# Kernel tuning notes

Hardware: AMD Instinct MI355X
Metric: run time of the kernel (lower is better)

Reference implementation:

```python
import jax, jax.numpy as jnp
import numpy as np

C, S, K, SIGMA = 512, 11, 3, 16
B = 128
EPS = 1e-5  # BatchNorm eps (eval mode, running_mean=0, running_var=1)


def _make_dct_weight(Cc, H, W):
    # FcaNet 'low16' frequency selection
    lx = [0, 0, 1, 1, 0, 2, 2, 1, 2, 0, 3, 4, 0, 1, 3, 0]
    ly = [0, 1, 0, 1, 2, 0, 1, 2, 2, 3, 0, 0, 4, 3, 1, 5]
    mx = [u * (H // 7) for u in lx]
    my = [v * (W // 7) for v in ly]
    w = np.zeros((Cc, H, W), np.float32)
    cp = Cc // len(lx)

    def bf(pos, freq, POS):
        r = np.cos(np.pi * freq * (pos + 0.5) / POS) / np.sqrt(POS)
        return r if freq == 0 else r * np.sqrt(2.0)

    for i, (u, v) in enumerate(zip(mx, my)):
        for tx in range(H):
            for ty in range(W):
                w[i * cp:(i + 1) * cp, tx, ty] = bf(tx, u, H) * bf(ty, v, W)
    return jnp.asarray(w)


def _bn(f, g, b):
    # eval-mode BatchNorm2d: (f - 0)/sqrt(1+eps)*g + b, per channel (axis 1)
    s = g / jnp.sqrt(1.0 + EPS)
    return f * s[None, :, None, None] + b[None, :, None, None]


def _conv1x1(f, w, b):
    return jnp.einsum('bchw,oc->bohw', f, w) + b[None, :, None, None]


def _spatial_kernel(f, w_conv, b_conv, g_sp, b_sp):
    Bn = f.shape[0]
    s = _conv1x1(f, w_conv, b_conv)                  # (B, K*K, S, S)
    s = s.reshape(Bn, K * K, S * S).transpose(0, 2, 1)  # (B, S*S, K*K)
    s = _bn(s.reshape(Bn, S * S, K, K), g_sp, b_sp)
    return s.reshape(Bn, S * S, K * K)


def _channel_kernel(f, dct_w, fc1, fc2, g_ch, b_ch):
    y = jnp.sum(f * dct_w[None], axis=(-2, -1))      # (B, C) DCT pooling
    y = jax.nn.sigmoid(jax.nn.relu(y @ fc1.T) @ fc2.T)  # (B, C*K*K)
    y = _bn(y.reshape(-1, C, K, K), g_ch, b_ch)
    return y.reshape(-1, C, K * K)


def _unfold(f):
    # torch-style per-pixel kxk neighborhoods -> (B, C, H, W, K, K)
    p = (K + 1) // 2 - 1
    Bn, Cn, H, W = f.shape
    fp = jnp.pad(f, ((0, 0), (0, 0), (p, p), (p, p)))
    pat = jnp.stack([fp[:, :, di:di + H, dj:dj + W]
                     for di in range(K) for dj in range(K)], axis=-1)
    return pat.reshape(Bn, Cn, H, W, K, K)


def setup_inputs() -> dict:
    key = jax.random.key(0)
    ks = iter(jax.random.split(key, 32))

    def nrm(shape, s=0.02):
        return s * jax.random.normal(next(ks), shape, jnp.float32)

    def gma(shape):
        return 1.0 + 0.1 * jax.random.normal(next(ks), shape, jnp.float32)

    return dict(
        x=jax.random.normal(next(ks), (B, C, S, S), jnp.float32),
        dct_w=_make_dct_weight(C, S, S),
        w_conv=nrm((K * K, C)), b_conv=nrm((K * K,)),
        g_sp=gma((S * S,)), b_sp=nrm((S * S,), 0.05),
        g_ch=gma((C,)), b_ch=nrm((C,), 0.05),
        fc1=nrm((C // SIGMA, C)), fc2=nrm((C * K * K, C // SIGMA)),
        up_w1=nrm((2 * C, C)), up_b1=nrm((2 * C,)), up_g1=gma((2 * C,)), up_bb1=nrm((2 * C,), 0.05),
        up_w2=nrm((2 * C, 2 * C)), up_b2=nrm((2 * C,)), up_g2=gma((2 * C,)), up_bb2=nrm((2 * C,), 0.05),
        lo_w1=nrm((2 * C, 2 * C)), lo_b1=nrm((2 * C,)), lo_g1=gma((2 * C,)), lo_bb1=nrm((2 * C,), 0.05),
        lo_w2=nrm((C, 2 * C)), lo_b2=nrm((C,)), lo_g2=gma((C,)), lo_bb2=nrm((C,), 0.05),
    )


def reference(x, dct_w, w_conv, b_conv, g_sp, b_sp, g_ch, b_ch, fc1, fc2,
              up_w1, up_b1, up_g1, up_bb1, up_w2, up_b2, up_g2, up_bb2,
              lo_w1, lo_b1, lo_g1, lo_bb1, lo_w2, lo_b2, lo_g2, lo_bb2):
    Bn = x.shape[0]
    # instance kernel: spatial (B,1,HW,KK) x channel (B,C,1,KK)
    sk = _spatial_kernel(x, w_conv, b_conv, g_sp, b_sp)[:, None]
    ck = _channel_kernel(x, dct_w, fc1, fc2, g_ch, b_ch)[:, :, None]
    inst = (sk * ck).reshape(Bn, C, S, S, K, K)
    # CLM task representation (sum over batch between upper and lower)
    a = jax.nn.relu(_bn(_conv1x1(x, up_w1, up_b1), up_g1, up_bb1))
    a = jax.nn.relu(_bn(_conv1x1(a, up_w2, up_b2), up_g2, up_bb2))
    a = a.sum(axis=0, keepdims=True)
    a = jax.nn.relu(_bn(_conv1x1(a, lo_w1, lo_b1), lo_g1, lo_bb1))
    task_s = jax.nn.sigmoid(_bn(_conv1x1(a, lo_w2, lo_b2), lo_g2, lo_bb2))
    # task kernel (shared across the batch)
    sk_t = _spatial_kernel(task_s, w_conv, b_conv, g_sp, b_sp)[:, None]
    ck_t = _channel_kernel(task_s, dct_w, fc1, fc2, g_ch, b_ch)[:, :, None]
    task_kernel = (sk_t * ck_t).reshape(1, C, S, S, K, K)
    kernel = task_kernel * inst
    adapted = (_unfold(x) * kernel).mean(axis=(-1, -2))  # (B,C,S,S)
    return adapted + x, task_kernel
```

## Files before the change

### kernel.cpp

```cpp
#include <hip/hip_runtime.h>
#include <hip/hip_bf16.h>
#include <math.h>

#define BNEPS 1e-5f
#define BDIM_B 128
#define CDIM 512
#define SS 121
#define KK 9
#define MROWS (BDIM_B * SS)

typedef unsigned short u16;
typedef __bf16 bf16x8 __attribute__((ext_vector_type(8)));
typedef float f32x4 __attribute__((ext_vector_type(4)));

__device__ __forceinline__ u16 f2bf(float f) {
    union { float f; unsigned int u; } v; v.f = f;
    unsigned int r = v.u + 0x7FFF + ((v.u >> 16) & 1);
    return (u16)(r >> 16);
}
__device__ __forceinline__ float bf2f(u16 v) {
    union { unsigned int u; float f; } x; x.u = ((unsigned int)v) << 16; return x.f;
}

__device__ __forceinline__ void gld16(const u16* g, u16* l) {
    __builtin_amdgcn_global_load_lds(
        (const __attribute__((address_space(1))) void*)g,
        (__attribute__((address_space(3))) void*)l, 16, 0, 0);
}

template<int MODE, int SWIZ>
__global__ __launch_bounds__(256)
void gemm_mfma(const u16* __restrict__ A, const u16* __restrict__ Bw,
               const float* __restrict__ bias, const float* __restrict__ g,
               const float* __restrict__ bb, void* __restrict__ out,
               int Kd, int N, int NT)
{
    __shared__ __align__(16) u16 Als[2][128 * 32];
    __shared__ __align__(16) u16 Bls[2][128 * 32];

    const int tid  = threadIdx.x;
    const int lane = tid & 63;
    const int w    = tid >> 6;
    const int wm   = w >> 1, wn = w & 1;

    int bx, by;
    if (SWIZ) {
        int i = blockIdx.x;
        if (i < 960) {
            int xg = i & 7;
            int j  = i >> 3;
            bx = xg * 15 + (j >> 3);
            by = j & 7;
        } else { bx = 120; by = i - 960; }
    } else {
        bx = blockIdx.x / NT; by = blockIdx.x - bx * NT;
    }
    const int bm = bx * 128;
    const int bn = by * 128;

    f32x4 acc[4][4] = {};

    const int subrow = tid >> 2;
    const int kq     = tid & 3;
    const int gchunk = kq ^ ((subrow >> 1) & 3);
    const u16* Ab = A  + (size_t)(bm + subrow) * Kd + gchunk * 8;
    const u16* Bb = Bw + (size_t)(bn + subrow) * Kd + gchunk * 8;
    u16* Al0  = &Als[0][(w * 16) * 32];
    u16* Al1  = &Als[0][(w * 16 + 64) * 32];
    u16* Bl0  = &Bls[0][(w * 16) * 32];
    u16* Bl1  = &Bls[0][(w * 16 + 64) * 32];
    u16* Al0b = &Als[1][(w * 16) * 32];
    u16* Al1b = &Als[1][(w * 16 + 64) * 32];
    u16* Bl0b = &Bls[1][(w * 16) * 32];
    u16* Bl1b = &Bls[1][(w * 16 + 64) * 32];

    const int fa_row = wm * 64 + (lane & 15);
    const int fb_row = wn * 64 + (lane & 15);
    const int kofs   = (((lane >> 4) ^ (((lane & 15) >> 1) & 3))) * 8;

    for (int k0 = 0; k0 < Kd; k0 += 64) {
        __syncthreads();
        gld16(Ab + k0,                      Al0);
        gld16(Ab + (size_t)64 * Kd + k0,    Al1);
        gld16(Bb + k0,                      Bl0);
        gld16(Bb + (size_t)64 * Kd + k0,    Bl1);
        gld16(Ab + k0 + 32,                 Al0b);
        gld16(Ab + (size_t)64 * Kd + k0 + 32, Al1b);
        gld16(Bb + k0 + 32,                 Bl0b);
        gld16(Bb + (size_t)64 * Kd + k0 + 32, Bl1b);
        __syncthreads();

        #pragma unroll
        for (int hb = 0; hb < 2; ++hb) {
            const u16* Ah = &Als[hb][0];
            const u16* Bh = &Bls[hb][0];
            bf16x8 af[4], bfv[4];
            #pragma unroll
            for (int i = 0; i < 4; ++i)
                af[i] = *(const bf16x8*)&Ah[(fa_row + i * 16) * 32 + kofs];
            #pragma unroll
            for (int j = 0; j < 4; ++j)
                bfv[j] = *(const bf16x8*)&Bh[(fb_row + j * 16) * 32 + kofs];
            #pragma unroll
            for (int i = 0; i < 4; ++i)
                #pragma unroll
                for (int j = 0; j < 4; ++j)
                    acc[i][j] = __builtin_amdgcn_mfma_f32_16x16x32_bf16(af[i], bfv[j], acc[i][j], 0, 0, 0);
        }
    }

    const float inv = 1.0f / sqrtf(1.0f + BNEPS);

    if (MODE == 1) {
        u16* Y = (u16*)out;
        int dstrow[4][4];
        #pragma unroll
        for (int i = 0; i < 4; ++i) {
            int mb = bm + wm * 64 + i * 16 + (lane >> 4) * 4;
            #pragma unroll
            for (int r = 0; r < 4; ++r) {
                int m = mb + r;
                int b = m / 121, p = m - b * 121;
                dstrow[i][r] = p * 128 + b;
            }
        }
        #pragma unroll
        for (int j = 0; j < 4; ++j) {
            int n = bn + wn * 64 + j * 16 + (lane & 15);
            float sc = g[n] * inv, bo = bias[n], bv = bb[n];
            #pragma unroll
            for (int i = 0; i < 4; ++i)
                #pragma unroll
                for (int r = 0; r < 4; ++r) {
                    float v = (acc[i][j][r] + bo) * sc + bv;
                    v = fmaxf(v, 0.0f);
                    Y[(size_t)dstrow[i][r] * N + n] = f2bf(v);
                }
        }
    } else {
        float ps[4];
        #pragma unroll
        for (int j = 0; j < 4; ++j) {
            int n = bn + wn * 64 + j * 16 + (lane & 15);
            float sc = g[n] * inv, bo = bias[n], bv = bb[n];
            float s = 0.f;
            #pragma unroll
            for (int i = 0; i < 4; ++i)
                #pragma unroll
                for (int r = 0; r < 4; ++r) {
                    float v = (acc[i][j][r] + bo) * sc + bv;
                    s += fmaxf(v, 0.0f);
                }
            ps[j] = s;
        }
        __syncthreads();
        float* red = (float*)Als;
        #pragma unroll
        for (int j = 0; j < 4; ++j)
            red[(wm * 4 + (lane >> 4)) * 128 + wn * 64 + j * 16 + (lane & 15)] = ps[j];
        __syncthreads();
        if (tid < 128) {
            float s = 0.f;
            #pragma unroll
            for (int r = 0; r < 8; ++r) s += red[r * 128 + tid];
            ((u16*)out)[(size_t)bx * N + bn + tid] = f2bf(s);
        }
    }
}

template<int MODE>
__global__ __launch_bounds__(256)
void gemm_small(const u16* __restrict__ A, const u16* __restrict__ Bw,
                const float* __restrict__ bias, const float* __restrict__ g,
                const float* __restrict__ bb, u16* __restrict__ Y,
                int Kd, int N)
{
    const int bn   = blockIdx.x * 64;
    const int tid  = threadIdx.x;
    const int lane = tid & 63;
    const int w    = tid >> 6;
    const int fr   = lane & 15;
    const int kq   = lane >> 4;
    const int r0   = w * 32;

    f32x4 acc[2][4] = {};
    const u16* a0p = A + (size_t)(r0 + fr) * Kd + kq * 8;
    const u16* a1p = a0p + (size_t)16 * Kd;
    const u16* bp  = Bw + (size_t)(bn + fr) * Kd + kq * 8;

    #pragma unroll 4
    for (int k0 = 0; k0 < Kd; k0 += 32) {
        bf16x8 a0 = *(const bf16x8*)(a0p + k0);
        bf16x8 a1 = *(const bf16x8*)(a1p + k0);
        #pragma unroll
        for (int j = 0; j < 4; ++j) {
            bf16x8 bv = *(const bf16x8*)(bp + (size_t)j * 16 * Kd + k0);
            acc[0][j] = __builtin_amdgcn_mfma_f32_16x16x32_bf16(a0, bv, acc[0][j], 0, 0, 0);
            acc[1][j] = __builtin_amdgcn_mfma_f32_16x16x32_bf16(a1, bv, acc[1][j], 0, 0, 0);
        }
    }

    const float inv = 1.0f / sqrtf(1.0f + BNEPS);
    #pragma unroll
    for (int j = 0; j < 4; ++j) {
        int n = bn + j * 16 + (lane & 15);
        float sc = g[n] * inv, bo = bias[n], bv = bb[n];
        #pragma unroll
        for (int t = 0; t < 2; ++t)
            #pragma unroll
            for (int r = 0; r < 4; ++r) {
                int m = r0 + t * 16 + (lane >> 4) * 4 + r;
                float v = (acc[t][j][r] + bo) * sc + bv;
                if (MODE == 3) v = fmaxf(v, 0.0f);
                else           v = 1.f / (1.f + expf(-v));
                Y[(size_t)m * N + n] = f2bf(v);
            }
    }
}

__device__ __forceinline__ void spatial_body(
    const u16* __restrict__ Arow, const u16* __restrict__ wcb,
    const float* __restrict__ b_conv, const float* __restrict__ g_sp,
    const float* __restrict__ b_sp, float* __restrict__ skb,
    bool task, int blk, float* __restrict__ skt)
{
    const float inv = 1.0f / sqrtf(1.0f + BNEPS);
    const int tid  = threadIdx.x;
    const int lane = tid & 63;
    const int w    = tid >> 6;
    const int fr   = lane & 15;
    const int kq   = lane >> 4;
    const int r0   = w * 32;

    f32x4 acc0 = {}, acc1 = {};
    const u16* a0p = Arow + (size_t)(r0 + fr) * 512 + kq * 8;
    const u16* a1p = a0p + (size_t)16 * 512;
    const u16* bp  = wcb + (size_t)fr * 512 + kq * 8;
    #pragma unroll
    for (int k0 = 0; k0 < 512; k0 += 32) {
        bf16x8 a0 = *(const bf16x8*)(a0p + k0);
        bf16x8 a1 = *(const bf16x8*)(a1p + k0);
        bf16x8 b  = *(const bf16x8*)(bp + k0);
        acc0 = __builtin_amdgcn_mfma_f32_16x16x32_bf16(a0, b, acc0, 0, 0, 0);
        acc1 = __builtin_amdgcn_mfma_f32_16x16x32_bf16(a1, b, acc1, 0, 0, 0);
    }

    int n = lane & 15;
    if (n < 9) {
        float bo = b_conv[n];
        #pragma unroll
        for (int t = 0; t < 2; ++t) {
            f32x4 a = t ? acc1 : acc0;
            #pragma unroll
            for (int r = 0; r < 4; ++r) {
                int mloc = r0 + t * 16 + (lane >> 4) * 4 + r;
                if (!task) {
                    int m = blk * 128 + mloc;
                    int p = m % 121;
                    float v = (a[r] + bo) * (g_sp[p] * inv) + b_sp[p];
                    skb[(size_t)m * 9 + n] = v;
                } else if (mloc < 121) {
                    float v = (a[r] + bo) * (g_sp[mloc] * inv) + b_sp[mloc];
                    skt[(size_t)mloc * 9 + n] = v;
                }
            }
        }
    }
}

__device__ __forceinline__ void channel_body(
    const u16* __restrict__ src, const float* __restrict__ dctT,
    const float* __restrict__ fc1, const float* __restrict__ fc2,
    const float* __restrict__ g_ch, const float* __restrict__ b_ch,
    float* __restrict__ outp, float* yls, float* y2ls)
{
    const float inv = 1.0f / sqrtf(1.0f + BNEPS);

    {
        int c = threadIdx.x * 2;
        float s0 = 0.f, s1 = 0.f;
        for (int p = 0; p < SS; ++p) {
            unsigned v = *(const unsigned*)(src + (size_t)p * 512 + c);
            float2 d  = *(const float2*)(dctT + (size_t)p * 512 + c);
            s0 += bf2f((u16)(v & 0xFFFFu)) * d.x;
            s1 += bf2f((u16)(v >> 16)) * d.y;
        }
        yls[c] = s0; yls[c + 1] = s1;
    }
    __syncthreads();

    {
        int o = threadIdx.x >> 3, kp = threadIdx.x & 7;
        const float* w = fc1 + (size_t)o * 512;
        float s = 0.f;
        for (int k = kp * 4; k < 512; k += 32) {
            float4 wv = *(const float4*)(w + k);
            float4 av = *(const float4*)(yls + k);
            s += wv.x * av.x + wv.y * av.y + wv.z * av.z + wv.w * av.w;
        }
        s += __shfl_xor(s, 1);
        s += __shfl_xor(s, 2);
        s += __shfl_xor(s, 4);
        if (kp == 0) y2ls[o] = fmaxf(s, 0.f);
    }
    __syncthreads();

    for (int o = threadIdx.x; o < CDIM * KK; o += 256) {
        const float* w = fc2 + (size_t)o * 32;
        float s = 0.f;
        #pragma unroll
        for (int k = 0; k < 32; ++k) s += y2ls[k] * w[k];
        s = 1.f / (1.f + expf(-s));
        int c = o / KK;
        s = s * (g_ch[c] * inv) + b_ch[c];
        outp[o] = s;
    }
}

__global__ __launch_bounds__(256)
void spatial_ck_combo(const u16* __restrict__ Xb, const u16* __restrict__ Xt,
                      const u16* __restrict__ wcb, const float* __restrict__ b_conv,
                      const float* __restrict__ g_sp, const float* __restrict__ b_sp,
                      const float* __restrict__ dctT,
                      const float* __restrict__ fc1, const float* __restrict__ fc2,
                      const float* __restrict__ g_ch, const float* __restrict__ b_ch,
                      float* __restrict__ skb, float* __restrict__ skt,
                      float* __restrict__ ckbuf, float* __restrict__ ck_t)
{
    __shared__ float sm[544];
    if (blockIdx.x < 122) {
        const bool task = (blockIdx.x == 121);
        spatial_body(task ? Xt : Xb + (size_t)blockIdx.x * 128 * 512,
                     wcb, b_conv, g_sp, b_sp, skb, task, blockIdx.x, skt);
        return;
    }
    const int g = blockIdx.x - 122;
    const u16* src = (g < 128) ? Xb + (size_t)g * 121 * 512 : Xt;
    channel_body(src, dctT, fc1, fc2, g_ch, b_ch,
                 (g < 128) ? ckbuf + (size_t)g * CDIM * KK : ck_t, sm, sm + 512);
}

#define W1N (1024 * 512)
#define W2N (1024 * 1024)
#define L1N (1024 * 1024)
#define L2N (512 * 1024)
#define VECN ((W1N + W2N + L1N + L2N) / 4)
#define DCTN (512 * 121)
#define WCN (16 * 512)
#define PREP_ELEM (VECN + DCTN + WCN)
#define PREP_BLKS (1024 + (PREP_ELEM + 255) / 256)
__global__ void prep_combo(const float* __restrict__ x, u16* __restrict__ Xb,
                           const float* __restrict__ w1, const float* __restrict__ w2,
                           const float* __restrict__ l1, const float* __restrict__ l2,
                           const float* __restrict__ dct, const float* __restrict__ w_conv,
                           u16* __restrict__ o1, u16* __restrict__ o2,
                           u16* __restrict__ o3, u16* __restrict__ o4,
                           float* __restrict__ dctT, u16* __restrict__ wcb)
{
    __shared__ float t[64 * 121];
    if (blockIdx.x < 1024) {
        int b = blockIdx.x >> 3, c0 = (blockIdx.x & 7) * 64;
        for (int idx = threadIdx.x; idx < 64 * 121; idx += 256) {
            int c = idx / 121, p = idx - c * 121;
            t[idx] = x[((size_t)b * 512 + c0 + c) * 121 + p];
        }
        __syncthreads();
        for (int idx = threadIdx.x; idx < 121 * 64; idx += 256) {
            int p = idx >> 6, c = idx & 63;
            Xb[((size_t)(b * 121 + p)) * 512 + c0 + c] = f2bf(t[c * 121 + p]);
        }
        return;
    }
    int i = (blockIdx.x - 1024) * 256 + threadIdx.x;
    if (i < VECN) {
        int q = i;
        const float* s; u16* d;
        if (q < W1N / 4)                    { s = w1; d = o1; }
        else if (q < (W1N + W2N) / 4)       { s = w2; d = o2; q -= W1N / 4; }
        else if (q < (W1N + W2N + L1N) / 4) { s = l1; d = o3; q -= (W1N + W2N) / 4; }
        else                                { s = l2; d = o4; q -= (W1N + W2N + L1N) / 4; }
        float4 v = ((const float4*)s)[q];
        uint2 r;
        r.x = (unsigned)f2bf(v.x) | ((unsigned)f2bf(v.y) << 16);
        r.y = (unsigned)f2bf(v.z) | ((unsigned)f2bf(v.w) << 16);
        ((uint2*)d)[q] = r;
        return;
    }
    i -= VECN;
    if (i < DCTN) {
        int p = i >> 9, c = i & 511;
        dctT[i] = dct[(size_t)c * 121 + p];
        return;
    }
    i -= DCTN;
    if (i < WCN) {
        int n = i >> 9, c = i & 511;
        wcb[i] = (n < 9) ? f2bf(w_conv[(size_t)n * 512 + c]) : (u16)0;
    }
}

#define TKN (CDIM * SS * KK)
#define FIN_BLKS (1024 + (TKN + 255) / 256)
__global__ __launch_bounds__(256)
void final_combo(const float* __restrict__ x, const float* __restrict__ skb,
                 const float* __restrict__ sk_t, const float* __restrict__ ckbuf,
                 const float* __restrict__ ck_t, float* __restrict__ out0,
                 float* __restrict__ tk)
{
    __shared__ float PS[SS * KK];
    __shared__ float CS[64 * KK];
    __shared__ float XT[64 * SS];

    if (blockIdx.x >= 1024) {
        int idx = (blockIdx.x - 1024) * 256 + threadIdx.x;
        if (idx < TKN) {
            int k9 = idx % KK;
            int pc = idx / KK;
            int p = pc % SS, c = pc / SS;
            tk[idx] = sk_t[p * KK + k9] * ck_t[c * KK + k9];
        }
        return;
    }

    const int tid = threadIdx.x;
    const int b = blockIdx.x >> 3, c0 = (blockIdx.x & 7) * 64;

    const float* sp = skb + (size_t)b * SS * KK;
    for (int i = tid; i < SS * KK; i += 256) PS[i] = sp[i] * sk_t[i];
    const float* cp = ckbuf + ((size_t)b * CDIM + c0) * KK;
    const float* tp = ck_t + (size_t)c0 * KK;
    for (int i = tid; i < (64 * KK) / 4; i += 256) {
        float4 a = ((const float4*)cp)[i];
        float4 bq = ((const float4*)tp)[i];
        float4 r; r.x = a.x * bq.x; r.y = a.y * bq.y; r.z = a.z * bq.z; r.w = a.w * bq.w;
        ((float4*)CS)[i] = r;
    }
    const float* xp = x + ((size_t)b * CDIM + c0) * SS;
    for (int i = tid; i < (64 * SS) / 4; i += 256)
        ((float4*)XT)[i] = ((const float4*)xp)[i];
    __syncthreads();

    float* op = out0 + ((size_t)b * CDIM + c0) * SS;
    for (int ci = tid; ci < (64 * SS) / 4; ci += 256) {
        float4 o;
        #pragma unroll
        for (int r = 0; r < 4; ++r) {
            int i = ci * 4 + r;
            int c = i / SS, p = i - c * SS;
            int h = p / 11, w = p - h * 11;
            const float* xc = XT + c * SS;
            const float* ps = PS + p * KK;
            const float* cs = CS + c * KK;
            float acc = 0.f;
            #pragma unroll
            for (int di = 0; di < 3; ++di) {
                int hh = h + di - 1;
                bool hv = (unsigned)hh < 11u;
                #pragma unroll
                for (int dj = 0; dj < 3; ++dj) {
                    int ww = w + dj - 1;
                    int k = di * 3 + dj;
                    float xv = (hv && (unsigned)ww < 11u) ? xc[hh * 11 + ww] : 0.f;
                    acc += xv * ps[k] * cs[k];
                }
            }
            ((float*)&o)[r] = acc * (1.0f / 9.0f) + xc[p];
        }
        ((float4*)op)[ci] = o;
    }
}

extern "C" void kernel_launch(void* const* d_in, const int* in_sizes, int n_in,
                              void* d_out, int out_size, void* d_ws, size_t ws_size,
                              hipStream_t stream)
{
    const float* x      = (const float*)d_in[0];
    const float* dct_w  = (const float*)d_in[1];
    const float* w_conv = (const float*)d_in[2];
    const float* b_conv = (const float*)d_in[3];
    const float* g_sp   = (const float*)d_in[4];
    const float* b_sp   = (const float*)d_in[5];
    const float* g_ch   = (const float*)d_in[6];
    const float* b_ch   = (const float*)d_in[7];
    const float* fc1    = (const float*)d_in[8];
    const float* fc2    = (const float*)d_in[9];
    const float* up_w1  = (const float*)d_in[10];
    const float* up_b1  = (const float*)d_in[11];
    const float* up_g1  = (const float*)d_in[12];
    const float* up_bb1 = (const float*)d_in[13];
    const float* up_w2  = (const float*)d_in[14];
    const float* up_b2  = (const float*)d_in[15];
    const float* up_g2  = (const float*)d_in[16];
    const float* up_bb2 = (const float*)d_in[17];
    const float* lo_w1  = (const float*)d_in[18];
    const float* lo_b1  = (const float*)d_in[19];
    const float* lo_g1  = (const float*)d_in[20];
    const float* lo_bb1 = (const float*)d_in[21];
    const float* lo_w2  = (const float*)d_in[22];
    const float* lo_b2  = (const float*)d_in[23];
    const float* lo_g2  = (const float*)d_in[24];
    const float* lo_bb2 = (const float*)d_in[25];

    float* out0 = (float*)d_out;
    float* tk   = out0 + (size_t)BDIM_B * CDIM * SS;

    char* ws = (char*)d_ws;
    size_t off = 0;
    auto alloc = [&](size_t bytes) { void* p = ws + off; off += (bytes + 63) & ~(size_t)63; return p; };
    u16*   Xb      = (u16*)alloc((size_t)MROWS * 512 * 2);
    u16*   Y1      = (u16*)alloc((size_t)MROWS * 1024 * 2);
    u16*   w1b     = (u16*)alloc((size_t)W1N * 2);
    u16*   w2b     = (u16*)alloc((size_t)W2N * 2);
    u16*   lw1b    = (u16*)alloc((size_t)L1N * 2);
    u16*   lw2b    = (u16*)alloc((size_t)L2N * 2);
    u16*   asum_b  = (u16*)alloc((size_t)128 * 1024 * 2);
    u16*   a3b     = (u16*)alloc((size_t)128 * 1024 * 2);
    u16*   ts_pc   = (u16*)alloc((size_t)128 * 512 * 2);
    float* dctT    = (float*)alloc((size_t)SS * 512 * 4);
    u16*   wcb     = (u16*)alloc((size_t)WCN * 2);
    float* ckbuf   = (float*)alloc((size_t)BDIM_B * CDIM * KK * 4);
    float* skbuf   = (float*)alloc((size_t)BDIM_B * SS * KK * 4);
    float* ck_t    = (float*)alloc((size_t)CDIM * KK * 4);
    float* sk_t    = (float*)alloc((size_t)SS * KK * 4);

    hipLaunchKernelGGL(prep_combo, dim3(PREP_BLKS), dim3(256), 0, stream,
                       x, Xb, up_w1, up_w2, lo_w1, lo_w2, dct_w, w_conv,
                       w1b, w2b, lw1b, lw2b, dctT, wcb);

    hipLaunchKernelGGL((gemm_mfma<1, 1>), dim3(121 * 8), dim3(256), 0, stream,
                       Xb, w1b, up_b1, up_g1, up_bb1, (void*)Y1, 512, 1024, 8);
    hipLaunchKernelGGL((gemm_mfma<2, 1>), dim3(121 * 8), dim3(256), 0, stream,
                       Y1, w2b, up_b2, up_g2, up_bb2, (void*)asum_b, 1024, 1024, 8);

    hipLaunchKernelGGL((gemm_small<3>), dim3(16), dim3(256), 0, stream,
                       asum_b, lw1b, lo_b1, lo_g1, lo_bb1, a3b, 1024, 1024);
    hipLaunchKernelGGL((gemm_small<4>), dim3(8), dim3(256), 0, stream,
                       a3b, lw2b, lo_b2, lo_g2, lo_bb2, ts_pc, 1024, 512);

    hipLaunchKernelGGL(spatial_ck_combo, dim3(122 + 129), dim3(256), 0, stream,
                       Xb, ts_pc, wcb, b_conv, g_sp, b_sp,
                       dctT, fc1, fc2, g_ch, b_ch,
                       skbuf, sk_t, ckbuf, ck_t);

    hipLaunchKernelGGL(final_combo, dim3(FIN_BLKS), dim3(256), 0, stream,
                       x, skbuf, sk_t, ckbuf, ck_t, out0, tk);
}
```

Measured before the change: 327.1 us.

## Fuse first GEMM with batch kernels; chain small lower GEMMs via grid barrier

The batch spatial and channel kernel computations now run as extra blocks in the same launch as the first large GEMM, since both depend only on Xb, so they fill the tail of that GEMM. The two small lower-branch GEMMs and the task spatial and channel kernels are merged into one 16-block kernel that uses an atomic grid barrier instead of separate launches. The barrier counter is reset inside the prep kernel. This removes several launches and serial gaps, but relies on all 16 blocks being resident at once for the spin barrier, and the heavier mixed blocks may disturb the GEMM's tile scheduling.

```diff
diff --git a/kernel.cpp b/kernel.cpp
--- a/kernel.cpp
+++ b/kernel.cpp
@@ -28,12 +28,12 @@
         (__attribute__((address_space(3))) void*)l, 16, 0, 0);
 }
 
-template<int MODE, int SWIZ>
-__global__ __launch_bounds__(256)
-void gemm_mfma(const u16* __restrict__ A, const u16* __restrict__ Bw,
-               const float* __restrict__ bias, const float* __restrict__ g,
-               const float* __restrict__ bb, void* __restrict__ out,
-               int Kd, int N, int NT)
+template<int MODE>
+__device__ __forceinline__ void gemm128_body(
+    const u16* __restrict__ A, const u16* __restrict__ Bw,
+    const float* __restrict__ bias, const float* __restrict__ g,
+    const float* __restrict__ bb, void* __restrict__ out,
+    int Kd, int N, int bi)
 {
     __shared__ __align__(16) u16 Als[2][128 * 32];
     __shared__ __align__(16) u16 Bls[2][128 * 32];
@@ -44,16 +44,14 @@
     const int wm   = w >> 1, wn = w & 1;
 
     int bx, by;
-    if (SWIZ) {
-        int i = blockIdx.x;
+    {
+        int i = bi;
         if (i < 960) {
             int xg = i & 7;
             int j  = i >> 3;
             bx = xg * 15 + (j >> 3);
             by = j & 7;
         } else { bx = 120; by = i - 960; }
-    } else {
-        bx = blockIdx.x / NT; by = blockIdx.x - bx * NT;
     }
     const int bm = bx * 128;
     const int bn = by * 128;
@@ -169,13 +167,12 @@
 }
 
 template<int MODE>
-__global__ __launch_bounds__(256)
-void gemm_small(const u16* __restrict__ A, const u16* __restrict__ Bw,
-                const float* __restrict__ bias, const float* __restrict__ g,
-                const float* __restrict__ bb, u16* __restrict__ Y,
-                int Kd, int N)
-{
-    const int bn   = blockIdx.x * 64;
+__device__ __forceinline__ void gemm_small_body(
+    const u16* __restrict__ A, const u16* __restrict__ Bw,
+    const float* __restrict__ bias, const float* __restrict__ g,
+    const float* __restrict__ bb, u16* __restrict__ Y,
+    int Kd, int N, int bn)
+{
     const int tid  = threadIdx.x;
     const int lane = tid & 63;
     const int w    = tid >> 6;
@@ -225,9 +222,8 @@
     bool task, int blk, float* __restrict__ skt)
 {
     const float inv = 1.0f / sqrtf(1.0f + BNEPS);
-    const int tid  = threadIdx.x;
-    const int lane = tid & 63;
-    const int w    = tid >> 6;
+    const int lane = threadIdx.x & 63;
+    const int w    = threadIdx.x >> 6;
     const int fr   = lane & 15;
     const int kq   = lane >> 4;
     const int r0   = w * 32;
@@ -317,27 +313,86 @@
     }
 }
 
+template<int MODE>
 __global__ __launch_bounds__(256)
-void spatial_ck_combo(const u16* __restrict__ Xb, const u16* __restrict__ Xt,
-                      const u16* __restrict__ wcb, const float* __restrict__ b_conv,
-                      const float* __restrict__ g_sp, const float* __restrict__ b_sp,
-                      const float* __restrict__ dctT,
-                      const float* __restrict__ fc1, const float* __restrict__ fc2,
-                      const float* __restrict__ g_ch, const float* __restrict__ b_ch,
-                      float* __restrict__ skb, float* __restrict__ skt,
-                      float* __restrict__ ckbuf, float* __restrict__ ck_t)
+void gemm_mfma(const u16* __restrict__ A, const u16* __restrict__ Bw,
+               const float* __restrict__ bias, const float* __restrict__ g,
+               const float* __restrict__ bb, void* __restrict__ out,
+               int Kd, int N)
+{
+    gemm128_body<MODE>(A, Bw, bias, g, bb, out, Kd, N, blockIdx.x);
+}
+
+__global__ __launch_bounds__(256)
+void mega1(const u16* __restrict__ Xb, const u16* __restrict__ w1b,
+           const float* __restrict__ up_b1, const float* __restrict__ up_g1,
+           const float* __restrict__ up_bb1, u16* __restrict__ Y1,
+           const u16* __restrict__ wcb, const float* __restrict__ b_conv,
+           const float* __restrict__ g_sp, const float* __restrict__ b_sp,
+           const float* __restrict__ dctT,
+           const float* __restrict__ fc1, const float* __restrict__ fc2,
+           const float* __restrict__ g_ch, const float* __restrict__ b_ch,
+           float* __restrict__ skb, float* __restrict__ ckbuf)
 {
     __shared__ float sm[544];
-    if (blockIdx.x < 122) {
-        const bool task = (blockIdx.x == 121);
-        spatial_body(task ? Xt : Xb + (size_t)blockIdx.x * 128 * 512,
-                     wcb, b_conv, g_sp, b_sp, skb, task, blockIdx.x, skt);
+    int bi = blockIdx.x;
+    if (bi < 968) {
+        gemm128_body<1>(Xb, w1b, up_b1, up_g1, up_bb1, (void*)Y1, 512, 1024, bi);
         return;
     }
-    const int g = blockIdx.x - 122;
-    const u16* src = (g < 128) ? Xb + (size_t)g * 121 * 512 : Xt;
-    channel_body(src, dctT, fc1, fc2, g_ch, b_ch,
-                 (g < 128) ? ckbuf + (size_t)g * CDIM * KK : ck_t, sm, sm + 512);
+    bi -= 968;
+    if (bi < 121) {
+        spatial_body(Xb + (size_t)bi * 128 * 512, wcb, b_conv, g_sp, b_sp,
+                     skb, false, bi, nullptr);
+        return;
+    }
+    bi -= 121;
+    channel_body(Xb + (size_t)bi * 121 * 512, dctT, fc1, fc2, g_ch, b_ch,
+                 ckbuf + (size_t)bi * CDIM * KK, sm, sm + 512);
+}
+
+__device__ __forceinline__ void gbar(int* bar, int target)
+{
+    __syncthreads();
+    if (threadIdx.x == 0) {
+        __threadfence();
+        atomicAdd(bar, 1);
+        while (atomicAdd(bar, 0) < target) { }
+        __threadfence();
+    }
+    __syncthreads();
+}
+
+__global__ __launch_bounds__(256)
+void lo_chain(const u16* __restrict__ asum_b, const u16* __restrict__ lw1b,
+              const float* __restrict__ lo_b1, const float* __restrict__ lo_g1,
+              const float* __restrict__ lo_bb1, u16* __restrict__ a3b,
+              const u16* __restrict__ lw2b,
+              const float* __restrict__ lo_b2, const float* __restrict__ lo_g2,
+              const float* __restrict__ lo_bb2, u16* __restrict__ ts_pc,
+              const u16* __restrict__ wcb, const float* __restrict__ b_conv,
+              const float* __restrict__ g_sp, const float* __restrict__ b_sp,
+              const float* __restrict__ dctT,
+              const float* __restrict__ fc1, const float* __restrict__ fc2,
+              const float* __restrict__ g_ch, const float* __restrict__ b_ch,
+              float* __restrict__ skt, float* __restrict__ ck_t,
+              int* __restrict__ bar)
+{
+    __shared__ float sm[544];
+
+    gemm_small_body<3>(asum_b, lw1b, lo_b1, lo_g1, lo_bb1, a3b, 1024, 1024,
+                       blockIdx.x * 64);
+    gbar(bar, 16);
+
+    if (blockIdx.x < 8)
+        gemm_small_body<4>(a3b, lw2b, lo_b2, lo_g2, lo_bb2, ts_pc, 1024, 512,
+                           blockIdx.x * 64);
+    gbar(bar, 32);
+
+    if (blockIdx.x == 0)
+        spatial_body(ts_pc, wcb, b_conv, g_sp, b_sp, nullptr, true, 0, skt);
+    else if (blockIdx.x == 1)
+        channel_body(ts_pc, dctT, fc1, fc2, g_ch, b_ch, ck_t, sm, sm + 512);
 }
 
 #define W1N (1024 * 512)
@@ -355,9 +410,11 @@
                            const float* __restrict__ dct, const float* __restrict__ w_conv,
                            u16* __restrict__ o1, u16* __restrict__ o2,
                            u16* __restrict__ o3, u16* __restrict__ o4,
-                           float* __restrict__ dctT, u16* __restrict__ wcb)
+                           float* __restrict__ dctT, u16* __restrict__ wcb,
+                           int* __restrict__ bar)
 {
     __shared__ float t[64 * 121];
+    if (blockIdx.x == 0 && threadIdx.x == 0) *bar = 0;
     if (blockIdx.x < 1024) {
         int b = blockIdx.x >> 3, c0 = (blockIdx.x & 7) * 64;
         for (int idx = threadIdx.x; idx < 64 * 121; idx += 256) {
@@ -522,25 +579,27 @@
     float* skbuf   = (float*)alloc((size_t)BDIM_B * SS * KK * 4);
     float* ck_t    = (float*)alloc((size_t)CDIM * KK * 4);
     float* sk_t    = (float*)alloc((size_t)SS * KK * 4);
+    int*   bar     = (int*)alloc(64);
 
     hipLaunchKernelGGL(prep_combo, dim3(PREP_BLKS), dim3(256), 0, stream,
                        x, Xb, up_w1, up_w2, lo_w1, lo_w2, dct_w, w_conv,
-                       w1b, w2b, lw1b, lw2b, dctT, wcb);
-
-    hipLaunchKernelGGL((gemm_mfma<1, 1>), dim3(121 * 8), dim3(256), 0, stream,
-                       Xb, w1b, up_b1, up_g1, up_bb1, (void*)Y1, 512, 1024, 8);
-    hipLaunchKernelGGL((gemm_mfma<2, 1>), dim3(121 * 8), dim3(256), 0, stream,
-                       Y1, w2b, up_b2, up_g2, up_bb2, (void*)asum_b, 1024, 1024, 8);
-
-    hipLaunchKernelGGL((gemm_small<3>), dim3(16), dim3(256), 0, stream,
-                       asum_b, lw1b, lo_b1, lo_g1, lo_bb1, a3b, 1024, 1024);
-    hipLaunchKernelGGL((gemm_small<4>), dim3(8), dim3(256), 0, stream,
-                       a3b, lw2b, lo_b2, lo_g2, lo_bb2, ts_pc, 1024, 512);
-
-    hipLaunchKernelGGL(spatial_ck_combo, dim3(122 + 129), dim3(256), 0, stream,
-                       Xb, ts_pc, wcb, b_conv, g_sp, b_sp,
+                       w1b, w2b, lw1b, lw2b, dctT, wcb, bar);
+
+    hipLaunchKernelGGL(mega1, dim3(968 + 121 + 128), dim3(256), 0, stream,
+                       Xb, w1b, up_b1, up_g1, up_bb1, Y1,
+                       wcb, b_conv, g_sp, b_sp,
                        dctT, fc1, fc2, g_ch, b_ch,
-                       skbuf, sk_t, ckbuf, ck_t);
+                       skbuf, ckbuf);
+
+    hipLaunchKernelGGL((gemm_mfma<2>), dim3(121 * 8), dim3(256), 0, stream,
+                       Y1, w2b, up_b2, up_g2, up_bb2, (void*)asum_b, 1024, 1024);
+
+    hipLaunchKernelGGL(lo_chain, dim3(16), dim3(256), 0, stream,
+                       asum_b, lw1b, lo_b1, lo_g1, lo_bb1, a3b,
+                       lw2b, lo_b2, lo_g2, lo_bb2, ts_pc,
+                       wcb, b_conv, g_sp, b_sp,
+                       dctT, fc1, fc2, g_ch, b_ch,
+                       sk_t, ck_t, bar);
 
     hipLaunchKernelGGL(final_combo, dim3(FIN_BLKS), dim3(256), 0, stream,
                        x, skbuf, sk_t, ckbuf, ck_t, out0, tk);
```

New measurement: 380.4 us. 1.16x slower.
